# Optimization experiments

Measured on AMD Instinct MI355X. Metric: run time of the kernel, lower is better.

Reference implementation:

```python
import jax, jax.numpy as jnp
import numpy as np
import math

B, S, C = 4, 2048, 128
H, DK, DV, K = 8, 64, 64, 3


def setup_inputs() -> dict:
    key = jax.random.key(0)
    ks = jax.random.split(key, 12)
    sd = 0.05
    return {
        "x": jax.random.normal(ks[0], (B, S, C), dtype=jnp.float32),
        "length": jax.random.randint(ks[1], (B,), 1, S + 1, dtype=jnp.int32),
        "wq": jax.random.normal(ks[2], (H * DK, C, K), dtype=jnp.float32) * sd,
        "bq": jnp.zeros((H * DK,), dtype=jnp.float32),
        "wk": jax.random.normal(ks[3], (H * DK, C, K), dtype=jnp.float32) * sd,
        "bk": jnp.zeros((H * DK,), dtype=jnp.float32),
        "wv": jax.random.normal(ks[4], (H * DV, C), dtype=jnp.float32) * sd,
        "bv": jnp.zeros((H * DV,), dtype=jnp.float32),
        "w1": jax.random.normal(ks[5], (DV, H * DV), dtype=jnp.float32) * sd,
        "b1": jnp.zeros((DV,), dtype=jnp.float32),
        "w2": jax.random.normal(ks[6], (1, DV), dtype=jnp.float32) * sd,
        "b2": jnp.zeros((1,), dtype=jnp.float32),
    }


def _causal_conv(x, w, b):
    # x: (b,s,c), w: (o,c,k) torch Conv1d layout -> (b,s,o), causal (left) padding
    y = jax.lax.conv_general_dilated(
        x.transpose(0, 2, 1), w, window_strides=(1,), padding=[(K - 1, 0)],
        dimension_numbers=("NCH", "OIH", "NCH"))
    return y.transpose(0, 2, 1) + b


def _split_heads(x, d):
    b, s, _ = x.shape
    return x.reshape(b, s, H, d).transpose(0, 2, 1, 3)  # (b,h,s,d)


def reference(x, length, wq, bq, wk, bk, wv, bv, w1, b1, w2, b2):
    q = _split_heads(_causal_conv(x, wq, bq), DK)            # (b,h,s,dk)
    k = _split_heads(_causal_conv(x, wk, bk), DK)            # (b,h,s,dk)
    v = _split_heads(jax.nn.relu(x @ wv.T + bv), DV)         # (b,h,s,dv)

    attn = jnp.einsum("bhqd,bhkd->bhqk", q, k) / math.sqrt(DK)
    # future mask: additive -1e9 above the diagonal (matches triu * -1e9 + softmax)
    future = jnp.triu(jnp.ones((S, S), dtype=attn.dtype), k=1) * (-1e9)
    score = jax.nn.softmax(attn + future, axis=-1)
    # padding mask: zero query rows >= length[b]
    row_valid = (jnp.arange(S)[None, :] < length[:, None]).astype(score.dtype)
    score = score * row_valid[:, None, :, None]              # (b,h,s,s)

    out1 = jnp.einsum("bhqk,bhkd->bhqd", score, v)           # (b,h,s,dv)
    out2 = out1.transpose(0, 2, 1, 3).reshape(x.shape[0], S, H * DV)
    out3 = jax.nn.relu(out2 @ w1.T + b1) @ w2.T + b2         # (b,s,1)
    return out3, score
```

## Files before the change

### kernel.cpp

```cpp
#include <hip/hip_runtime.h>

#define S_ 2048
#define C_ 128
#define B_ 4
#define H_ 8
#define D_ 64

typedef __attribute__((ext_vector_type(8))) short bf16x8;
typedef __attribute__((ext_vector_type(4))) float f32x4;

__device__ inline unsigned short f2bf(float f) {
    union { float f; unsigned int u; } c; c.f = f;
    unsigned int u = c.u;
    unsigned int r = (u + 0x7FFFu + ((u >> 16) & 1u)) >> 16;
    return (unsigned short)r;
}
__device__ inline float bf2f(unsigned short s) {
    union { unsigned int u; float f; } c; c.u = ((unsigned int)s) << 16;
    return c.f;
}

__global__ __launch_bounds__(256) void prep_kernel(
    const float* __restrict__ x,
    const float* __restrict__ wq, const float* __restrict__ wk,
    const float* __restrict__ wv, const float* __restrict__ w1,
    unsigned short* __restrict__ xh,
    unsigned short* __restrict__ wPackQ, unsigned short* __restrict__ wPackK,
    unsigned short* __restrict__ wPackV, float* __restrict__ w1T)
{
    int idx = blockIdx.x * 256 + threadIdx.x;
    if (idx < 1048576) {
        xh[idx] = f2bf(x[idx]);
    } else if (idx < 1245184) {
        int i = idx - 1048576;
        int t = i >> 16, r = i & 65535;
        int o = r >> 7, c = r & 127;
        wPackQ[i] = f2bf(wq[o * 384 + c * 3 + t]);
    } else if (idx < 1441792) {
        int i = idx - 1245184;
        int t = i >> 16, r = i & 65535;
        int o = r >> 7, c = r & 127;
        wPackK[i] = f2bf(wk[o * 384 + c * 3 + t]);
    } else if (idx < 1507328) {
        int i = idx - 1441792;
        wPackV[i] = f2bf(wv[i]);
    } else if (idx < 1540096) {
        int i = idx - 1507328;
        int j = i >> 6, d = i & 63;
        w1T[i] = w1[d * 512 + j];
    }
}

__global__ __launch_bounds__(256) void qkv_kernel(
    const unsigned short* __restrict__ xh,
    const unsigned short* __restrict__ wPackQ, const unsigned short* __restrict__ wPackK,
    const unsigned short* __restrict__ wPackV,
    const float* __restrict__ bq, const float* __restrict__ bk,
    const float* __restrict__ bv,
    unsigned short* __restrict__ Qh, unsigned short* __restrict__ Kh,
    unsigned short* __restrict__ VhT)
{
    __shared__ __align__(16) short xs[130 * 136];
    __shared__ __align__(16) short ws[64 * 136];

    int s0 = blockIdx.x * 128;
    int h = blockIdx.y;
    int b = blockIdx.z;
    int bh = b * H_ + h;
    int tid = threadIdx.x;
    int w = tid >> 6;
    int lane = tid & 63;
    int col = lane & 15;
    int quad = lane >> 4;

    for (int i = tid; i < 2080; i += 256) {
        int row = i >> 4, c8 = (i & 15) << 3;
        int s = s0 - 2 + row;
        uint4 v = {0u, 0u, 0u, 0u};
        if (s >= 0) v = *(const uint4*)&xh[((long)b * S_ + s) * C_ + c8];
        *(uint4*)&xs[row * 136 + c8] = v;
    }

    for (int sec = 0; sec < 3; sec++) {
        const unsigned short* wsel = (sec == 0) ? wPackQ : (sec == 1) ? wPackK : wPackV;
        int tlo = (sec == 2) ? 2 : 0;

        f32x4 acc[2][4];
        #pragma unroll
        for (int rt = 0; rt < 2; rt++)
            #pragma unroll
            for (int nt = 0; nt < 4; nt++) acc[rt][nt] = (f32x4){0.f, 0.f, 0.f, 0.f};

        for (int t = tlo; t < 3; t++) {
            if (!(sec == 0 && t == 0)) __syncthreads();
            long wbase = (sec == 2) ? ((long)h * 8192)
                                    : ((long)t * 65536 + (long)h * 8192);
            for (int i = tid; i < 1024; i += 256) {
                int row = i >> 4, c8 = (i & 15) << 3;
                *(uint4*)&ws[row * 136 + c8] = *(const uint4*)&wsel[wbase + row * 128 + c8];
            }
            __syncthreads();

            #pragma unroll
            for (int kc = 0; kc < 4; kc++) {
                int ko = kc * 32 + quad * 8;
                bf16x8 a0 = *(const bf16x8*)&xs[(w * 32 + col + t) * 136 + ko];
                bf16x8 a1 = *(const bf16x8*)&xs[(w * 32 + 16 + col + t) * 136 + ko];
                #pragma unroll
                for (int nt = 0; nt < 4; nt++) {
                    bf16x8 bfr = *(const bf16x8*)&ws[(nt * 16 + col) * 136 + ko];
                    acc[0][nt] = __builtin_amdgcn_mfma_f32_16x16x32_bf16(a0, bfr, acc[0][nt], 0, 0, 0);
                    acc[1][nt] = __builtin_amdgcn_mfma_f32_16x16x32_bf16(a1, bfr, acc[1][nt], 0, 0, 0);
                }
            }
        }

        if (sec == 0) {
            #pragma unroll
            for (int nt = 0; nt < 4; nt++) {
                float bias = bq[h * 64 + nt * 16 + col];
                #pragma unroll
                for (int rt = 0; rt < 2; rt++)
                    #pragma unroll
                    for (int r = 0; r < 4; r++) {
                        int s = s0 + w * 32 + rt * 16 + quad * 4 + r;
                        Qh[((long)bh * S_ + s) * D_ + nt * 16 + col] =
                            f2bf((acc[rt][nt][r] + bias) * 0.125f);
                    }
            }
        } else if (sec == 1) {
            #pragma unroll
            for (int nt = 0; nt < 4; nt++) {
                float bias = bk[h * 64 + nt * 16 + col];
                #pragma unroll
                for (int rt = 0; rt < 2; rt++)
                    #pragma unroll
                    for (int r = 0; r < 4; r++) {
                        int s = s0 + w * 32 + rt * 16 + quad * 4 + r;
                        Kh[((long)bh * S_ + s) * D_ + nt * 16 + col] =
                            f2bf(acc[rt][nt][r] + bias);
                    }
            }
        } else {
            __syncthreads();
            #pragma unroll
            for (int nt = 0; nt < 4; nt++) {
                float bias = bv[h * 64 + nt * 16 + col];
                #pragma unroll
                for (int rt = 0; rt < 2; rt++)
                    #pragma unroll
                    for (int r = 0; r < 4; r++) {
                        int sl = w * 32 + rt * 16 + quad * 4 + r;
                        ws[(nt * 16 + col) * 136 + sl] =
                            (short)f2bf(fmaxf(acc[rt][nt][r] + bias, 0.f));
                    }
            }
            __syncthreads();
            for (int i = tid; i < 1024; i += 256) {
                int row = i >> 4, c8 = (i & 15) << 3;
                *(uint4*)&VhT[((long)bh * D_ + row) * S_ + s0 + c8] =
                    *(const uint4*)&ws[row * 136 + c8];
            }
        }
    }
}

#define PST 78
__global__ __launch_bounds__(256) void attn_kernel(
    const unsigned short* __restrict__ Qh, const unsigned short* __restrict__ Kh,
    const unsigned short* __restrict__ VhT, const int* __restrict__ length,
    float* __restrict__ score, float* __restrict__ out2)
{
    __shared__ __align__(16) short Kbuf[2][64 * 72];
    __shared__ __align__(16) short Pfh[64 * PST];

    int idx = blockIdx.x;
    int xcd = idx & 7;
    int slot = idx >> 3;
    int t = slot >> 2;
    int qt = (t < 16) ? t : 47 - t;
    int bh = xcd * 4 + (slot & 3);
    int b = bh >> 3, h = bh & 7;
    int q0 = qt * 64;
    int tid = threadIdx.x;
    int w = tid >> 6;
    int lane = tid & 63;
    int col = lane & 15;
    int quad = lane >> 4;
    int len = length[b];

    const unsigned short* Qb = Qh + (long)bh * S_ * D_;
    const unsigned short* Kb = Kh + (long)bh * S_ * D_;
    const unsigned short* Vtb = VhT + (long)bh * D_ * S_;
    float* scb = score + (long)bh * S_ * S_;

    int srow_ = tid >> 2, sc16_ = (tid & 3) * 16;

    {
        *(uint4*)&Pfh[srow_ * PST + sc16_]     = *(const uint4*)&Qb[(q0 + srow_) * D_ + sc16_];
        *(uint4*)&Pfh[srow_ * PST + sc16_ + 8] = *(const uint4*)&Qb[(q0 + srow_) * D_ + sc16_ + 8];
    }
    __syncthreads();
    int arow = w * 16 + col;
    bf16x8 aq0 = *(const bf16x8*)&Pfh[arow * PST + quad * 8];
    bf16x8 aq1 = *(const bf16x8*)&Pfh[arow * PST + 32 + quad * 8];

    float lrun[4];
    #pragma unroll
    for (int r = 0; r < 4; r++) lrun[r] = 0.f;

    {
        *(uint4*)&Kbuf[0][srow_ * 72 + sc16_]     = *(const uint4*)&Kb[srow_ * D_ + sc16_];
        *(uint4*)&Kbuf[0][srow_ * 72 + sc16_ + 8] = *(const uint4*)&Kb[srow_ * D_ + sc16_ + 8];
    }
    __syncthreads();

    for (int kt = 0; kt <= qt; kt++) {
        int buf = kt & 1;
        if (kt < qt) {
            *(uint4*)&Kbuf[1 - buf][srow_ * 72 + sc16_] =
                *(const uint4*)&Kb[((kt + 1) * 64 + srow_) * D_ + sc16_];
            *(uint4*)&Kbuf[1 - buf][srow_ * 72 + sc16_ + 8] =
                *(const uint4*)&Kb[((kt + 1) * 64 + srow_) * D_ + sc16_ + 8];
        }

        f32x4 acc[4];
        #pragma unroll
        for (int n = 0; n < 4; n++) acc[n] = (f32x4){0.f, 0.f, 0.f, 0.f};
        #pragma unroll
        for (int n = 0; n < 4; n++) {
            bf16x8 b0 = *(const bf16x8*)&Kbuf[buf][(n * 16 + col) * 72 + quad * 8];
            acc[n] = __builtin_amdgcn_mfma_f32_16x16x32_bf16(aq0, b0, acc[n], 0, 0, 0);
            bf16x8 b1 = *(const bf16x8*)&Kbuf[buf][(n * 16 + col) * 72 + 32 + quad * 8];
            acc[n] = __builtin_amdgcn_mfma_f32_16x16x32_bf16(aq1, b1, acc[n], 0, 0, 0);
        }
        if (kt == qt) {
            #pragma unroll
            for (int n = 0; n < 4; n++) {
                int kk = kt * 64 + n * 16 + col;
                #pragma unroll
                for (int r = 0; r < 4; r++) {
                    int q = q0 + w * 16 + quad * 4 + r;
                    if (kk > q) acc[n][r] = -1.0e30f;
                }
            }
        }
        #pragma unroll
        for (int r = 0; r < 4; r++) {
            lrun[r] += __expf(acc[0][r]) + __expf(acc[1][r]) +
                       __expf(acc[2][r]) + __expf(acc[3][r]);
        }
        __syncthreads();
    }

    #pragma unroll
    for (int off = 1; off < 16; off <<= 1) {
        #pragma unroll
        for (int r = 0; r < 4; r++) lrun[r] += __shfl_xor(lrun[r], off, 64);
    }
    float linv[4];
    #pragma unroll
    for (int r = 0; r < 4; r++) linv[r] = 1.0f / lrun[r];

    f32x4 oacc[4];
    #pragma unroll
    for (int n = 0; n < 4; n++) oacc[n] = (f32x4){0.f, 0.f, 0.f, 0.f};

    for (int kt = 0; kt <= qt; kt++) {
        __syncthreads();
        {
            *(uint4*)&Kbuf[0][srow_ * 72 + sc16_] =
                *(const uint4*)&Kb[(kt * 64 + srow_) * D_ + sc16_];
            *(uint4*)&Kbuf[0][srow_ * 72 + sc16_ + 8] =
                *(const uint4*)&Kb[(kt * 64 + srow_) * D_ + sc16_ + 8];
            *(uint4*)&Kbuf[1][srow_ * 72 + sc16_] =
                *(const uint4*)&Vtb[srow_ * S_ + kt * 64 + sc16_];
            *(uint4*)&Kbuf[1][srow_ * 72 + sc16_ + 8] =
                *(const uint4*)&Vtb[srow_ * S_ + kt * 64 + sc16_ + 8];
        }
        __syncthreads();

        f32x4 acc[4];
        #pragma unroll
        for (int n = 0; n < 4; n++) acc[n] = (f32x4){0.f, 0.f, 0.f, 0.f};
        #pragma unroll
        for (int n = 0; n < 4; n++) {
            bf16x8 b0 = *(const bf16x8*)&Kbuf[0][(n * 16 + col) * 72 + quad * 8];
            acc[n] = __builtin_amdgcn_mfma_f32_16x16x32_bf16(aq0, b0, acc[n], 0, 0, 0);
            bf16x8 b1 = *(const bf16x8*)&Kbuf[0][(n * 16 + col) * 72 + 32 + quad * 8];
            acc[n] = __builtin_amdgcn_mfma_f32_16x16x32_bf16(aq1, b1, acc[n], 0, 0, 0);
        }

        bool diag = (kt == qt);
        #pragma unroll
        for (int n = 0; n < 4; n++) {
            int kk = kt * 64 + n * 16 + col;
            #pragma unroll
            for (int r = 0; r < 4; r++) {
                int q = q0 + w * 16 + quad * 4 + r;
                float p = __expf(acc[n][r]) * linv[r];
                if (q >= len || (diag && kk > q)) p = 0.f;
                Pfh[(w * 16 + quad * 4 + r) * PST + n * 16 + col] = (short)f2bf(p);
            }
        }
        bf16x8 pa0 = *(const bf16x8*)&Pfh[(w * 16 + col) * PST + quad * 8];
        bf16x8 pa1 = *(const bf16x8*)&Pfh[(w * 16 + col) * PST + 32 + quad * 8];
        #pragma unroll
        for (int n = 0; n < 4; n++) {
            bf16x8 v0 = *(const bf16x8*)&Kbuf[1][(n * 16 + col) * 72 + quad * 8];
            oacc[n] = __builtin_amdgcn_mfma_f32_16x16x32_bf16(pa0, v0, oacc[n], 0, 0, 0);
            bf16x8 v1 = *(const bf16x8*)&Kbuf[1][(n * 16 + col) * 72 + 32 + quad * 8];
            oacc[n] = __builtin_amdgcn_mfma_f32_16x16x32_bf16(pa1, v1, oacc[n], 0, 0, 0);
        }

        {
            int rlo = lane >> 4;
            int c4 = (lane & 15) * 4;
            #pragma unroll
            for (int j = 0; j < 4; j++) {
                int row = w * 16 + j * 4 + rlo;
                uint2 pk = *(const uint2*)&Pfh[row * PST + c4];
                f32x4 v;
                v[0] = bf2f((unsigned short)(pk.x & 0xFFFFu));
                v[1] = bf2f((unsigned short)(pk.x >> 16));
                v[2] = bf2f((unsigned short)(pk.y & 0xFFFFu));
                v[3] = bf2f((unsigned short)(pk.y >> 16));
                __builtin_nontemporal_store(v,
                    (f32x4*)&scb[(long)(q0 + row) * S_ + kt * 64 + c4]);
            }
        }
    }

    #pragma unroll
    for (int n = 0; n < 4; n++) {
        #pragma unroll
        for (int r = 0; r < 4; r++) {
            int q = q0 + w * 16 + quad * 4 + r;
            out2[((long)(b * S_ + q)) * 512 + h * 64 + n * 16 + col] = oacc[n][r];
        }
    }

    f32x4 z = (f32x4){0.f, 0.f, 0.f, 0.f};
    for (int kt2 = qt + 1; kt2 < 32; kt2++) {
        #pragma unroll
        for (int it = 0; it < 4; it++) {
            int idx2 = tid + it * 256;
            int rr = idx2 >> 4, cc = idx2 & 15;
            __builtin_nontemporal_store(z,
                (f32x4*)&scb[(long)(q0 + rr) * S_ + kt2 * 64 + cc * 4]);
        }
    }
}

__global__ __launch_bounds__(256) void mlp_kernel(
    const float* __restrict__ out2, const float* __restrict__ w1T,
    const float* __restrict__ b1, const float* __restrict__ w2,
    const float* __restrict__ b2, float* __restrict__ out3)
{
    __shared__ float xr[2048];
    int sg0 = blockIdx.x * 4;
    int tid = threadIdx.x;
    for (int i = tid; i < 2048; i += 256) xr[i] = out2[(long)sg0 * 512 + i];
    __syncthreads();

    int sl = tid >> 6, d = tid & 63;
    float acc = 0.f;
    const float* xp = &xr[sl * 512];
    #pragma unroll 8
    for (int j = 0; j < 512; j++) acc += xp[j] * w1T[j * 64 + d];
    float hval = fmaxf(acc + b1[d], 0.f);
    float p = hval * w2[d];
    #pragma unroll
    for (int off = 32; off > 0; off >>= 1) p += __shfl_xor(p, off, 64);
    if (d == 0) out3[sg0 + sl] = p + b2[0];
}

extern "C" void kernel_launch(void* const* d_in, const int* in_sizes, int n_in,
                              void* d_out, int out_size, void* d_ws, size_t ws_size,
                              hipStream_t stream) {
    const float* x      = (const float*)d_in[0];
    const int*   length = (const int*)  d_in[1];
    const float* wq     = (const float*)d_in[2];
    const float* bq     = (const float*)d_in[3];
    const float* wk     = (const float*)d_in[4];
    const float* bk     = (const float*)d_in[5];
    const float* wv     = (const float*)d_in[6];
    const float* bv     = (const float*)d_in[7];
    const float* w1     = (const float*)d_in[8];
    const float* b1     = (const float*)d_in[9];
    const float* w2     = (const float*)d_in[10];
    const float* b2     = (const float*)d_in[11];

    float* out3  = (float*)d_out;
    float* score = (float*)d_out + 8192;

    float* ws  = (float*)d_ws;
    unsigned short* xh     = (unsigned short*)ws;  ws += 524288;
    unsigned short* wPackQ = (unsigned short*)ws;  ws += 98304;
    unsigned short* wPackK = (unsigned short*)ws;  ws += 98304;
    unsigned short* wPackV = (unsigned short*)ws;  ws += 32768;
    float* w1T = ws;  ws += 32768;
    unsigned short* Qh  = (unsigned short*)ws;  ws += 2097152;
    unsigned short* Kh  = (unsigned short*)ws;  ws += 2097152;
    unsigned short* VhT = (unsigned short*)ws;  ws += 2097152;
    float* o2  = ws;  ws += 4194304;

    hipLaunchKernelGGL(prep_kernel, dim3(6016), dim3(256), 0, stream,
                       x, wq, wk, wv, w1, xh, wPackQ, wPackK, wPackV, w1T);
    hipLaunchKernelGGL(qkv_kernel, dim3(16, 8, 4), dim3(256), 0, stream,
                       xh, wPackQ, wPackK, wPackV, bq, bk, bv, Qh, Kh, VhT);
    hipLaunchKernelGGL(attn_kernel, dim3(1024), dim3(256), 0, stream,
                       Qh, Kh, VhT, length, score, o2);
    hipLaunchKernelGGL(mlp_kernel, dim3(2048), dim3(256), 0, stream,
                       o2, w1T, b1, w2, b2, out3);
}
```

Baseline: 657.7 us.

## Register-prefetch K/V tiles, use exp2 softmax, pack bf16 P, and vectorize MLP

Several changes at once. The attention kernel loads K/V tiles into registers one iteration ahead and writes them to LDS afterwards, which overlaps global latency and removes a sync in the stats pass. Q is read straight into registers, and log2(e) is folded into the Q scale so exp2f can replace __expf. P is converted with v_cvt_pk_bf16_f32, and launch bounds ask for 4 blocks per CU. The MLP reads w1 rows directly with float4 vector loads instead of using a transposed copy, which drops that work from prep. Possible risks are more register pressure and per-thread strided w1 reads.

```diff
diff --git a/kernel.cpp b/kernel.cpp
--- a/kernel.cpp
+++ b/kernel.cpp
@@ -23,10 +23,10 @@
 __global__ __launch_bounds__(256) void prep_kernel(
     const float* __restrict__ x,
     const float* __restrict__ wq, const float* __restrict__ wk,
-    const float* __restrict__ wv, const float* __restrict__ w1,
+    const float* __restrict__ wv,
     unsigned short* __restrict__ xh,
     unsigned short* __restrict__ wPackQ, unsigned short* __restrict__ wPackK,
-    unsigned short* __restrict__ wPackV, float* __restrict__ w1T)
+    unsigned short* __restrict__ wPackV)
 {
     int idx = blockIdx.x * 256 + threadIdx.x;
     if (idx < 1048576) {
@@ -44,10 +44,6 @@
     } else if (idx < 1507328) {
         int i = idx - 1441792;
         wPackV[i] = f2bf(wv[i]);
-    } else if (idx < 1540096) {
-        int i = idx - 1507328;
-        int j = i >> 6, d = i & 63;
-        w1T[i] = w1[d * 512 + j];
     }
 }
 
@@ -125,7 +121,7 @@
                     for (int r = 0; r < 4; r++) {
                         int s = s0 + w * 32 + rt * 16 + quad * 4 + r;
                         Qh[((long)bh * S_ + s) * D_ + nt * 16 + col] =
-                            f2bf((acc[rt][nt][r] + bias) * 0.125f);
+                            f2bf((acc[rt][nt][r] + bias) * 0.18033688011112042f);
                     }
             }
         } else if (sec == 1) {
@@ -166,7 +162,7 @@
 }
 
 #define PST 78
-__global__ __launch_bounds__(256) void attn_kernel(
+__global__ __launch_bounds__(256, 4) void attn_kernel(
     const unsigned short* __restrict__ Qh, const unsigned short* __restrict__ Kh,
     const unsigned short* __restrict__ VhT, const int* __restrict__ length,
     float* __restrict__ score, float* __restrict__ out2)
@@ -196,32 +192,26 @@
 
     int srow_ = tid >> 2, sc16_ = (tid & 3) * 16;
 
-    {
-        *(uint4*)&Pfh[srow_ * PST + sc16_]     = *(const uint4*)&Qb[(q0 + srow_) * D_ + sc16_];
-        *(uint4*)&Pfh[srow_ * PST + sc16_ + 8] = *(const uint4*)&Qb[(q0 + srow_) * D_ + sc16_ + 8];
-    }
-    __syncthreads();
     int arow = w * 16 + col;
-    bf16x8 aq0 = *(const bf16x8*)&Pfh[arow * PST + quad * 8];
-    bf16x8 aq1 = *(const bf16x8*)&Pfh[arow * PST + 32 + quad * 8];
+    bf16x8 aq0 = *(const bf16x8*)&Qb[(q0 + arow) * D_ + quad * 8];
+    bf16x8 aq1 = *(const bf16x8*)&Qb[(q0 + arow) * D_ + 32 + quad * 8];
 
     float lrun[4];
     #pragma unroll
     for (int r = 0; r < 4; r++) lrun[r] = 0.f;
 
-    {
-        *(uint4*)&Kbuf[0][srow_ * 72 + sc16_]     = *(const uint4*)&Kb[srow_ * D_ + sc16_];
-        *(uint4*)&Kbuf[0][srow_ * 72 + sc16_ + 8] = *(const uint4*)&Kb[srow_ * D_ + sc16_ + 8];
-    }
+    uint4 k0, k1, v0, v1;
+    k0 = *(const uint4*)&Kb[srow_ * D_ + sc16_];
+    k1 = *(const uint4*)&Kb[srow_ * D_ + sc16_ + 8];
+    *(uint4*)&Kbuf[0][srow_ * 72 + sc16_]     = k0;
+    *(uint4*)&Kbuf[0][srow_ * 72 + sc16_ + 8] = k1;
     __syncthreads();
 
     for (int kt = 0; kt <= qt; kt++) {
         int buf = kt & 1;
         if (kt < qt) {
-            *(uint4*)&Kbuf[1 - buf][srow_ * 72 + sc16_] =
-                *(const uint4*)&Kb[((kt + 1) * 64 + srow_) * D_ + sc16_];
-            *(uint4*)&Kbuf[1 - buf][srow_ * 72 + sc16_ + 8] =
-                *(const uint4*)&Kb[((kt + 1) * 64 + srow_) * D_ + sc16_ + 8];
+            k0 = *(const uint4*)&Kb[((kt + 1) * 64 + srow_) * D_ + sc16_];
+            k1 = *(const uint4*)&Kb[((kt + 1) * 64 + srow_) * D_ + sc16_ + 8];
         }
 
         f32x4 acc[4];
@@ -247,10 +237,14 @@
         }
         #pragma unroll
         for (int r = 0; r < 4; r++) {
-            lrun[r] += __expf(acc[0][r]) + __expf(acc[1][r]) +
-                       __expf(acc[2][r]) + __expf(acc[3][r]);
-        }
-        __syncthreads();
+            lrun[r] += exp2f(acc[0][r]) + exp2f(acc[1][r]) +
+                       exp2f(acc[2][r]) + exp2f(acc[3][r]);
+        }
+        if (kt < qt) {
+            *(uint4*)&Kbuf[1 - buf][srow_ * 72 + sc16_]     = k0;
+            *(uint4*)&Kbuf[1 - buf][srow_ * 72 + sc16_ + 8] = k1;
+            __syncthreads();
+        }
     }
 
     #pragma unroll
@@ -266,19 +260,25 @@
     #pragma unroll
     for (int n = 0; n < 4; n++) oacc[n] = (f32x4){0.f, 0.f, 0.f, 0.f};
 
+    k0 = *(const uint4*)&Kb[srow_ * D_ + sc16_];
+    k1 = *(const uint4*)&Kb[srow_ * D_ + sc16_ + 8];
+    v0 = *(const uint4*)&Vtb[srow_ * S_ + sc16_];
+    v1 = *(const uint4*)&Vtb[srow_ * S_ + sc16_ + 8];
+
+    int prow = w * 16 + quad * 4;
     for (int kt = 0; kt <= qt; kt++) {
         __syncthreads();
-        {
-            *(uint4*)&Kbuf[0][srow_ * 72 + sc16_] =
-                *(const uint4*)&Kb[(kt * 64 + srow_) * D_ + sc16_];
-            *(uint4*)&Kbuf[0][srow_ * 72 + sc16_ + 8] =
-                *(const uint4*)&Kb[(kt * 64 + srow_) * D_ + sc16_ + 8];
-            *(uint4*)&Kbuf[1][srow_ * 72 + sc16_] =
-                *(const uint4*)&Vtb[srow_ * S_ + kt * 64 + sc16_];
-            *(uint4*)&Kbuf[1][srow_ * 72 + sc16_ + 8] =
-                *(const uint4*)&Vtb[srow_ * S_ + kt * 64 + sc16_ + 8];
-        }
+        *(uint4*)&Kbuf[0][srow_ * 72 + sc16_]     = k0;
+        *(uint4*)&Kbuf[0][srow_ * 72 + sc16_ + 8] = k1;
+        *(uint4*)&Kbuf[1][srow_ * 72 + sc16_]     = v0;
+        *(uint4*)&Kbuf[1][srow_ * 72 + sc16_ + 8] = v1;
         __syncthreads();
+        if (kt < qt) {
+            k0 = *(const uint4*)&Kb[((kt + 1) * 64 + srow_) * D_ + sc16_];
+            k1 = *(const uint4*)&Kb[((kt + 1) * 64 + srow_) * D_ + sc16_ + 8];
+            v0 = *(const uint4*)&Vtb[srow_ * S_ + (kt + 1) * 64 + sc16_];
+            v1 = *(const uint4*)&Vtb[srow_ * S_ + (kt + 1) * 64 + sc16_ + 8];
+        }
 
         f32x4 acc[4];
         #pragma unroll
@@ -295,22 +295,32 @@
         #pragma unroll
         for (int n = 0; n < 4; n++) {
             int kk = kt * 64 + n * 16 + col;
+            float p[4];
             #pragma unroll
             for (int r = 0; r < 4; r++) {
-                int q = q0 + w * 16 + quad * 4 + r;
-                float p = __expf(acc[n][r]) * linv[r];
-                if (q >= len || (diag && kk > q)) p = 0.f;
-                Pfh[(w * 16 + quad * 4 + r) * PST + n * 16 + col] = (short)f2bf(p);
-            }
-        }
+                int q = q0 + prow + r;
+                float pv = exp2f(acc[n][r]) * linv[r];
+                if (q >= len || (diag && kk > q)) pv = 0.f;
+                p[r] = pv;
+            }
+            unsigned int pk01, pk23;
+            asm("v_cvt_pk_bf16_f32 %0, %1, %2" : "=v"(pk01) : "v"(p[0]), "v"(p[1]));
+            asm("v_cvt_pk_bf16_f32 %0, %1, %2" : "=v"(pk23) : "v"(p[2]), "v"(p[3]));
+            int pcol = n * 16 + col;
+            Pfh[prow * PST + pcol]       = (short)(pk01 & 0xFFFFu);
+            Pfh[(prow + 1) * PST + pcol] = (short)(pk01 >> 16);
+            Pfh[(prow + 2) * PST + pcol] = (short)(pk23 & 0xFFFFu);
+            Pfh[(prow + 3) * PST + pcol] = (short)(pk23 >> 16);
+        }
+
         bf16x8 pa0 = *(const bf16x8*)&Pfh[(w * 16 + col) * PST + quad * 8];
         bf16x8 pa1 = *(const bf16x8*)&Pfh[(w * 16 + col) * PST + 32 + quad * 8];
         #pragma unroll
         for (int n = 0; n < 4; n++) {
-            bf16x8 v0 = *(const bf16x8*)&Kbuf[1][(n * 16 + col) * 72 + quad * 8];
-            oacc[n] = __builtin_amdgcn_mfma_f32_16x16x32_bf16(pa0, v0, oacc[n], 0, 0, 0);
-            bf16x8 v1 = *(const bf16x8*)&Kbuf[1][(n * 16 + col) * 72 + 32 + quad * 8];
-            oacc[n] = __builtin_amdgcn_mfma_f32_16x16x32_bf16(pa1, v1, oacc[n], 0, 0, 0);
+            bf16x8 vv0 = *(const bf16x8*)&Kbuf[1][(n * 16 + col) * 72 + quad * 8];
+            oacc[n] = __builtin_amdgcn_mfma_f32_16x16x32_bf16(pa0, vv0, oacc[n], 0, 0, 0);
+            bf16x8 vv1 = *(const bf16x8*)&Kbuf[1][(n * 16 + col) * 72 + 32 + quad * 8];
+            oacc[n] = __builtin_amdgcn_mfma_f32_16x16x32_bf16(pa1, vv1, oacc[n], 0, 0, 0);
         }
 
         {
@@ -353,7 +363,7 @@
 }
 
 __global__ __launch_bounds__(256) void mlp_kernel(
-    const float* __restrict__ out2, const float* __restrict__ w1T,
+    const float* __restrict__ out2, const float* __restrict__ w1,
     const float* __restrict__ b1, const float* __restrict__ w2,
     const float* __restrict__ b2, float* __restrict__ out3)
 {
@@ -364,10 +374,15 @@
     __syncthreads();
 
     int sl = tid >> 6, d = tid & 63;
+    const float* xp = &xr[sl * 512];
+    const float* wp = &w1[d * 512];
     float acc = 0.f;
-    const float* xp = &xr[sl * 512];
-    #pragma unroll 8
-    for (int j = 0; j < 512; j++) acc += xp[j] * w1T[j * 64 + d];
+    #pragma unroll 4
+    for (int j = 0; j < 512; j += 4) {
+        f32x4 xv = *(const f32x4*)&xp[j];
+        f32x4 wv = *(const f32x4*)&wp[j];
+        acc += xv[0] * wv[0] + xv[1] * wv[1] + xv[2] * wv[2] + xv[3] * wv[3];
+    }
     float hval = fmaxf(acc + b1[d], 0.f);
     float p = hval * w2[d];
     #pragma unroll
@@ -399,18 +414,17 @@
     unsigned short* wPackQ = (unsigned short*)ws;  ws += 98304;
     unsigned short* wPackK = (unsigned short*)ws;  ws += 98304;
     unsigned short* wPackV = (unsigned short*)ws;  ws += 32768;
-    float* w1T = ws;  ws += 32768;
     unsigned short* Qh  = (unsigned short*)ws;  ws += 2097152;
     unsigned short* Kh  = (unsigned short*)ws;  ws += 2097152;
     unsigned short* VhT = (unsigned short*)ws;  ws += 2097152;
     float* o2  = ws;  ws += 4194304;
 
-    hipLaunchKernelGGL(prep_kernel, dim3(6016), dim3(256), 0, stream,
-                       x, wq, wk, wv, w1, xh, wPackQ, wPackK, wPackV, w1T);
+    hipLaunchKernelGGL(prep_kernel, dim3(5888), dim3(256), 0, stream,
+                       x, wq, wk, wv, xh, wPackQ, wPackK, wPackV);
     hipLaunchKernelGGL(qkv_kernel, dim3(16, 8, 4), dim3(256), 0, stream,
                        xh, wPackQ, wPackK, wPackV, bq, bk, bv, Qh, Kh, VhT);
     hipLaunchKernelGGL(attn_kernel, dim3(1024), dim3(256), 0, stream,
                        Qh, Kh, VhT, length, score, o2);
     hipLaunchKernelGGL(mlp_kernel, dim3(2048), dim3(256), 0, stream,
-                       o2, w1T, b1, w2, b2, out3);
-}
+                       o2, w1, b1, w2, b2, out3);
+}
```

After: 731.8 us. +11.3%, slower.
